# Performance work log

Hardware: AMD Instinct MI355X
Metric: run time of the kernel (lower is better)

## Reference

```python
import jax, jax.numpy as jnp
import numpy as np

# dims
B, C, LM, LE, D, R, P, M, NL = 64, 16, 40, 32, 768, 2048, 49, 4, 2
COS_EPS = 1e-8
# fixed graph topology from GCNLayer: vertexes = [mention_text, mention_image, entity_text, entity_image]
VERTEX_GRAPH = [[(0, 2), (1, 3)], [(2, 2), (3, 3)], [(0, 0), (2, 1)], [(1, 0), (3, 1)]]
EDGE_GRAPH = [(0, 2), (0, 3), (1, 2), (1, 3)]


def _cos(x, y):
    # torch.nn.CosineSimilarity(dim=-1): dot / max(|x|*|y|, eps)
    num = jnp.sum(x * y, axis=-1)
    den = jnp.sqrt(jnp.sum(x * x, axis=-1)) * jnp.sqrt(jnp.sum(y * y, axis=-1))
    return num / jnp.maximum(den, COS_EPS)


def _span_mean(feat, start, end):
    # mean of token features over [start, end] inclusive  (mention final repr)
    pos = jnp.arange(feat.shape[1])
    m = ((pos >= start[:, None]) & (pos <= end[:, None])).astype(feat.dtype)[..., None]
    return (feat * m).sum(1) / jnp.maximum(m.sum(1), 1e-9)


def _ln(x, g, b):
    mu = jnp.mean(x, axis=-1, keepdims=True)
    var = jnp.mean((x - mu) ** 2, axis=-1, keepdims=True)
    return (x - mu) / jnp.sqrt(var + 1e-5) * g + b


def setup_inputs() -> dict:
    key = jax.random.key(0)
    ks = jax.random.split(key, 32)
    n = lambda i, shape, s=1.0: jax.random.normal(ks[i], shape, jnp.float32) * s
    start = jax.random.randint(ks[20], (B,), 0, 16)
    end = start + jax.random.randint(ks[21], (B,), 1, 16)
    return {
        "mention_text_feature": n(0, (B, LM, D)),
        "mention_text_mask": jnp.ones((B, LM), jnp.int32),
        "mention_start_pos": start,
        "mention_end_pos": end,
        "mention_image_feature": n(1, (B, P, R)),
        "mention_object_feature": n(2, (B, M, R)),
        "mention_object_score": jax.random.uniform(ks[22], (B, M), jnp.float32),
        "entity_text_feature": n(3, (B, C, LE, D)),
        "entity_text_mask": jnp.ones((B, C, LE), jnp.int32),
        "entity_image_feature": n(4, (B, C, P, R)),
        "entity_object_feature": n(5, (B, C, M, R)),
        "entity_object_score": jax.random.uniform(ks[23], (B, C, M), jnp.float32),
        "miet_similarity": n(6, (B, C)),
        "mtei_similarity": n(7, (B, C)),
        "w_mt": n(8, (D, D), 0.02), "b_mt": jnp.zeros((D,), jnp.float32),
        "w_et": n(9, (D, D), 0.02), "b_et": jnp.zeros((D,), jnp.float32),
        "w_mi": n(10, (R, D), 0.02), "b_mi": jnp.zeros((D,), jnp.float32),
        "w_ei": n(11, (R, D), 0.02), "b_ei": jnp.zeros((D,), jnp.float32),
        "wh_w": n(12, (NL, D, D), 0.02), "wh_b": jnp.zeros((NL, D), jnp.float32),
        "wu_w": n(13, (NL, D, D), 0.02), "wu_b": jnp.zeros((NL, D), jnp.float32),
        "wv_w": n(14, (NL, D, D), 0.02), "wv_b": jnp.zeros((NL, D), jnp.float32),
        "ln_g": jnp.ones((NL, D), jnp.float32), "ln_b": jnp.zeros((NL, D), jnp.float32),
    }


def reference(mention_text_feature, mention_text_mask, mention_start_pos, mention_end_pos,
              mention_image_feature, mention_object_feature, mention_object_score,
              entity_text_feature, entity_text_mask, entity_image_feature,
              entity_object_feature, entity_object_score, miet_similarity, mtei_similarity,
              w_mt, b_mt, w_et, b_et, w_mi, b_mi, w_ei, b_ei,
              wh_w, wh_b, wu_w, wu_b, wv_w, wv_b, ln_g, ln_b):
    # ---------------- VertexEncoder ----------------
    span = _span_mean(mention_text_feature, mention_start_pos, mention_end_pos)        # [B, D]
    v0 = span @ w_mt + b_mt                                                            # mention text  [B, D]
    em = entity_text_mask.astype(jnp.float32)[..., None]                               # [B, C, LE, 1]
    ent_rep = (entity_text_feature * em).sum(2) / jnp.maximum(em.sum(2), 1e-9)         # [B, C, D]
    v2 = ent_rep @ w_et + b_et                                                         # entity text   [B, C, D]
    v1 = mention_image_feature.mean(1) @ w_mi + b_mi                                   # mention image [B, D]
    v3 = entity_image_feature.mean(2) @ w_ei + b_ei                                    # entity image  [B, C, D]
    # ---------------- EdgeEncoder ----------------
    mtet = _cos(span[:, None, :], entity_text_feature[:, :, 0])                        # [B, C]
    # pairwise object cosine: vectorized over the torch double loop
    dots = jnp.einsum('bmr,bcnr->bcmn', mention_object_feature, entity_object_feature)
    nm = jnp.sqrt(jnp.sum(mention_object_feature ** 2, -1))                            # [B, M]
    ne = jnp.sqrt(jnp.sum(entity_object_feature ** 2, -1))                             # [B, C, M]
    sim = dots / jnp.maximum(nm[:, None, :, None] * ne[:, :, None, :], COS_EPS)        # [B, C, M, M]
    score = mention_object_score[:, None, :, None] * entity_object_score[:, :, None, :]
    miei = (sim * score).sum((-2, -1)) / (score.sum((-2, -1)) + 1e-9)                  # [B, C]
    # scaler edges (gcn_edge_enabled = all ones)
    edges = [mtet, mtei_similarity / 100.0, miet_similarity / 100.0, miei]
    vertexes = [v0, v1, v2, v3]
    # ---------------- GCN layers ----------------
    def conv_v(e, v):
        # scaler edge e: [B, C];  v is [B, C, D] (entity) or [B, D] (mention)
        if v.ndim == 3:
            return jnp.mean(e[:, :, None] * v, axis=1)          # -> [B, D]
        return e[:, :, None] * v[:, None, :]                    # -> [B, C, D]

    for l in range(NL):
        wh, bh = wh_w[l], wh_b[l]
        wu, bu = wu_w[l], wu_b[l]
        wv, bv = wv_w[l], wv_b[l]
        g, bln = ln_g[l], ln_b[l]
        new_v = []
        for u, nbrs in zip(vertexes, VERTEX_GRAPH):
            s = u
            for ei, vi in nbrs:
                s = s + conv_v(edges[ei], vertexes[vi])
            new_v.append(jax.nn.relu(_ln(s @ wh + bh, g, bln)))
        new_e = []
        for e, (ui, vi) in zip(edges, EDGE_GRAPH):
            fu = (vertexes[ui] @ wu + bu)[:, None, :]           # [B, 1, D]
            fv = vertexes[vi] @ wv + bv                         # [B, C, D]
            ne2 = jnp.mean(fu * fv, axis=-1)                    # [B, C]
            new_e.append(jax.nn.relu(ne2 + e))                  # w_m = Identity in scaler mode
        vertexes, edges = new_v, new_e
    # ---------------- output ----------------
    return _cos(vertexes[0][:, None, :], vertexes[2])           # [B, C]
```

## Files before the change

kernel.cpp:

```cpp
#include <hip/hip_runtime.h>

#define DIMB 64
#define DIMC 16
#define DIMLM 40
#define DIMLE 32
#define DIMD 768
#define DIMR 2048
#define DIMP 49
#define BC (DIMB * DIMC)

typedef __attribute__((ext_vector_type(8))) short short8;
typedef __attribute__((ext_vector_type(4))) float f32x4;

__device__ __forceinline__ float warpSum(float v) {
  v += __shfl_down(v, 32); v += __shfl_down(v, 16); v += __shfl_down(v, 8);
  v += __shfl_down(v, 4);  v += __shfl_down(v, 2);  v += __shfl_down(v, 1);
  return v;
}

__device__ __forceinline__ float blockSum256(float v, float* buf) {
  v = warpSum(v);
  int lane = threadIdx.x & 63, wid = threadIdx.x >> 6;
  if (lane == 0) buf[wid] = v;
  __syncthreads();
  float s = buf[0] + buf[1] + buf[2] + buf[3];
  __syncthreads();
  return s;
}

__device__ __forceinline__ void splitf(float x, unsigned short& h, unsigned short& l) {
  unsigned bx = __float_as_uint(x);
  h = (unsigned short)(bx >> 16);
  float lo = x - __uint_as_float(bx & 0xffff0000u);
  unsigned bl = __float_as_uint(lo);
  l = (unsigned short)((bl + 0x7fffu + ((bl >> 16) & 1u)) >> 16);
}

__global__ void k_span(const float* __restrict__ mtf, const int* __restrict__ st,
                       const int* __restrict__ en, float* __restrict__ outp) {
  int b = blockIdx.x;
  int s = st[b], e = en[b];
  float cnt = 0.0f;
  for (int p = 0; p < DIMLM; ++p) cnt += (p >= s && p <= e) ? 1.0f : 0.0f;
  float den = fmaxf(cnt, 1e-9f);
  for (int d = threadIdx.x; d < DIMD; d += 256) {
    float acc = 0.0f;
    for (int p = s; p <= e && p < DIMLM; ++p)
      acc += mtf[((size_t)b * DIMLM + p) * DIMD + d];
    outp[b * DIMD + d] = acc / den;
  }
}

__global__ void k_entrep(const float* __restrict__ etf, const int* __restrict__ etm,
                         float* __restrict__ outp) {
  int bc = blockIdx.x;
  const float4* f = (const float4*)(etf + (size_t)bc * DIMLE * DIMD);
  const int* mk = etm + bc * DIMLE;
  float cnt = 0.0f;
  for (int l = 0; l < DIMLE; ++l) cnt += (float)mk[l];
  float rden = 1.0f / fmaxf(cnt, 1e-9f);
  for (int d4 = threadIdx.x; d4 < DIMD / 4; d4 += 256) {
    float sx = 0, sy = 0, sz = 0, sw = 0;
    for (int l = 0; l < DIMLE; ++l) {
      float m = (float)mk[l];
      float4 v = f[(size_t)l * (DIMD / 4) + d4];
      sx += v.x * m; sy += v.y * m; sz += v.z * m; sw += v.w * m;
    }
    float4 o = { sx * rden, sy * rden, sz * rden, sw * rden };
    ((float4*)(outp + (size_t)bc * DIMD))[d4] = o;
  }
}

__global__ void k_pmean(const float* __restrict__ in, float* __restrict__ outp, int np) {
  int row = blockIdx.y;
  int r4 = blockIdx.x * 256 + threadIdx.x;
  const float4* p = (const float4*)(in + (size_t)row * np * DIMR) + r4;
  float sx = 0, sy = 0, sz = 0, sw = 0;
  for (int i = 0; i < np; ++i) {
    float4 v = p[(size_t)i * (DIMR / 4)];
    sx += v.x; sy += v.y; sz += v.z; sw += v.w;
  }
  float rn = 1.0f / (float)np;
  float4 o = { sx * rn, sy * rn, sz * rn, sw * rn };
  ((float4*)(outp + (size_t)row * DIMR))[r4] = o;
}

__global__ void k_mtet(const float* __restrict__ span, const float* __restrict__ etf,
                       float* __restrict__ e0) {
  __shared__ float buf[4];
  int bc = blockIdx.x, b = bc >> 4;
  const float* x = span + b * DIMD;
  const float* y = etf + (size_t)bc * DIMLE * DIMD;
  float dot = 0, nx = 0, ny = 0;
  for (int d = threadIdx.x; d < DIMD; d += 256) {
    float xv = x[d], yv = y[d];
    dot += xv * yv; nx += xv * xv; ny += yv * yv;
  }
  dot = blockSum256(dot, buf);
  nx = blockSum256(nx, buf);
  ny = blockSum256(ny, buf);
  if (threadIdx.x == 0) e0[bc] = dot / fmaxf(sqrtf(nx) * sqrtf(ny), 1e-8f);
}

__global__ void k_einit(const float* __restrict__ mtei, const float* __restrict__ miet,
                        float* __restrict__ e1, float* __restrict__ e2) {
  int i = blockIdx.x * 256 + threadIdx.x;
  if (i < BC) { e1[i] = mtei[i] * 0.01f; e2[i] = miet[i] * 0.01f; }
}

__global__ void k_miei(const float* __restrict__ mof, const float* __restrict__ eof,
                       const float* __restrict__ mos, const float* __restrict__ eos,
                       float* __restrict__ e3) {
  __shared__ float red[24][4];
  int bc = blockIdx.x, b = bc >> 4;
  const float* mop = mof + (size_t)b * 4 * DIMR;
  const float* eop = eof + (size_t)bc * 4 * DIMR;
  float dots[16] = {}; float nm2[4] = {}; float ne2[4] = {};
  for (int r = threadIdx.x; r < DIMR; r += 256) {
    float mv[4], ev[4];
#pragma unroll
    for (int m = 0; m < 4; ++m) mv[m] = mop[(size_t)m * DIMR + r];
#pragma unroll
    for (int n = 0; n < 4; ++n) ev[n] = eop[(size_t)n * DIMR + r];
#pragma unroll
    for (int m = 0; m < 4; ++m) {
      nm2[m] += mv[m] * mv[m];
#pragma unroll
      for (int n = 0; n < 4; ++n) dots[m * 4 + n] += mv[m] * ev[n];
    }
#pragma unroll
    for (int n = 0; n < 4; ++n) ne2[n] += ev[n] * ev[n];
  }
  int lane = threadIdx.x & 63, wid = threadIdx.x >> 6;
#pragma unroll
  for (int i = 0; i < 24; ++i) {
    float v = (i < 16) ? dots[i] : (i < 20 ? nm2[i - 16] : ne2[i - 20]);
    v = warpSum(v);
    if (lane == 0) red[i][wid] = v;
  }
  __syncthreads();
  if (threadIdx.x == 0) {
    float dsum[16], nmv[4], nev[4];
    for (int i = 0; i < 16; ++i) dsum[i] = red[i][0] + red[i][1] + red[i][2] + red[i][3];
    for (int m = 0; m < 4; ++m)
      nmv[m] = sqrtf(red[16 + m][0] + red[16 + m][1] + red[16 + m][2] + red[16 + m][3]);
    for (int n = 0; n < 4; ++n)
      nev[n] = sqrtf(red[20 + n][0] + red[20 + n][1] + red[20 + n][2] + red[20 + n][3]);
    float num = 0, den = 0;
    for (int m = 0; m < 4; ++m)
      for (int n = 0; n < 4; ++n) {
        float sim = dsum[m * 4 + n] / fmaxf(nmv[m] * nev[n], 1e-8f);
        float sc = mos[b * 4 + m] * eos[bc * 4 + n];
        num += sim * sc; den += sc;
      }
    e3[bc] = num / (den + 1e-9f);
  }
}

struct WDesc { const float* W; unsigned short* Th; unsigned short* Tl; int K; };
struct WDescs { WDesc d[10]; };
__global__ void k_wsplitT(WDescs wd) {
  const WDesc D = wd.d[blockIdx.z];
  int kb = blockIdx.x * 32;
  if (kb >= D.K) return;
  int nb = blockIdx.y * 32;
  __shared__ float t[32][33];
  int c = threadIdx.x & 31, r8 = threadIdx.x >> 5;
#pragma unroll
  for (int i = 0; i < 4; ++i) {
    int kk = r8 + i * 8;
    t[kk][c] = D.W[(size_t)(kb + kk) * DIMD + nb + c];
  }
  __syncthreads();
#pragma unroll
  for (int i = 0; i < 4; ++i) {
    int nn = r8 + i * 8;
    unsigned short h, l;
    splitf(t[c][nn], h, l);
    size_t o = (size_t)(nb + nn) * D.K + kb + c;
    D.Th[o] = h; D.Tl[o] = l;
  }
}

struct ADesc { const float* X; unsigned short* H; unsigned short* L; };
struct ADescs { ADesc d[4]; int cum[5]; int nd; };
__global__ void k_asplit(ADescs ad) {
  int i4 = blockIdx.x * 256 + threadIdx.x;
  for (int z = 0; z < ad.nd; ++z) {
    if (i4 < ad.cum[z + 1]) {
      int off = i4 - ad.cum[z];
      const ADesc D = ad.d[z];
      float4 v = ((const float4*)D.X)[off];
      unsigned short h0, h1, h2, h3, l0, l1, l2, l3;
      splitf(v.x, h0, l0); splitf(v.y, h1, l1);
      splitf(v.z, h2, l2); splitf(v.w, h3, l3);
      uint2 hp, lp;
      hp.x = (unsigned)h0 | ((unsigned)h1 << 16); hp.y = (unsigned)h2 | ((unsigned)h3 << 16);
      lp.x = (unsigned)l0 | ((unsigned)l1 << 16); lp.y = (unsigned)l2 | ((unsigned)l3 << 16);
      ((uint2*)D.H)[off] = hp;
      ((uint2*)D.L)[off] = lp;
      return;
    }
  }
}

#define BMg 128
#define BNg 128
#define BKg 32
#define LDP 40
struct GDesc {
  const unsigned short *Ah, *Al, *Wh, *Wl;
  const float* bias; float* C; int M, K, mb0;
};
struct GDescs { GDesc d[4]; int nd; };

__global__ __launch_bounds__(256) void k_gemm_mfma(GDescs gd) {
  int bx = blockIdx.x;
  int z = 0;
  while (z + 1 < gd.nd && bx >= gd.d[z + 1].mb0) ++z;
  const GDesc D = gd.d[z];
  const int m0 = (bx - D.mb0) * BMg;
  const int n0 = blockIdx.y * BNg;
  const int K = D.K, M = D.M;

  __shared__ unsigned short sAh[2][BMg * LDP];
  __shared__ unsigned short sAl[2][BMg * LDP];
  __shared__ unsigned short sWh[2][BMg * LDP];
  __shared__ unsigned short sWl[2][BMg * LDP];

  const int tid = threadIdx.x;
  uint4 st[8];

  auto issue = [&](int kt) {
    int k0 = kt * BKg;
#pragma unroll
    for (int i = 0; i < 8; ++i) {
      int u = tid + (i & 1) * 256;
      int r = u >> 2, q = u & 3;
      const unsigned short* src;
      int row;
      if (i < 4) { row = m0 + r; if (row >= M) row = M - 1; src = (i < 2) ? D.Ah : D.Al; }
      else       { row = n0 + r;                            src = (i < 6) ? D.Wh : D.Wl; }
      st[i] = *(const uint4*)(src + (size_t)row * K + k0 + q * 8);
    }
  };
  auto commit = [&](int b) {
#pragma unroll
    for (int i = 0; i < 8; ++i) {
      int u = tid + (i & 1) * 256;
      int r = u >> 2, q = u & 3;
      unsigned short* dst = (i < 2) ? sAh[b] : (i < 4) ? sAl[b] : (i < 6) ? sWh[b] : sWl[b];
      *(uint4*)(dst + r * LDP + q * 8) = st[i];
    }
  };

  f32x4 acc[4][4];
#pragma unroll
  for (int i = 0; i < 4; ++i)
#pragma unroll
    for (int j = 0; j < 4; ++j) acc[i][j] = (f32x4){0.f, 0.f, 0.f, 0.f};

  const int lane = tid & 63, w = tid >> 6;
  const int wr = (w >> 1) * 64, wc = (w & 1) * 64;
  const int fr = lane & 15, fg = lane >> 4;

  issue(0); commit(0); __syncthreads();
  const int nt = K / BKg;
  for (int t = 0; t < nt; ++t) {
    int b = t & 1;
    if (t + 1 < nt) issue(t + 1);
    short8 ah[4], al[4];
#pragma unroll
    for (int mi = 0; mi < 4; ++mi) {
      int ro = (wr + mi * 16 + fr) * LDP + fg * 8;
      ah[mi] = *(const short8*)(sAh[b] + ro);
      al[mi] = *(const short8*)(sAl[b] + ro);
    }
#pragma unroll
    for (int ni = 0; ni < 4; ++ni) {
      int co = (wc + ni * 16 + fr) * LDP + fg * 8;
      short8 wh8 = *(const short8*)(sWh[b] + co);
      short8 wl8 = *(const short8*)(sWl[b] + co);
#pragma unroll
      for (int mi = 0; mi < 4; ++mi) {
        acc[mi][ni] = __builtin_amdgcn_mfma_f32_16x16x32_bf16(ah[mi], wh8, acc[mi][ni], 0, 0, 0);
        acc[mi][ni] = __builtin_amdgcn_mfma_f32_16x16x32_bf16(ah[mi], wl8, acc[mi][ni], 0, 0, 0);
        acc[mi][ni] = __builtin_amdgcn_mfma_f32_16x16x32_bf16(al[mi], wh8, acc[mi][ni], 0, 0, 0);
      }
    }
    if (t + 1 < nt) commit((t + 1) & 1);
    __syncthreads();
  }

#pragma unroll
  for (int mi = 0; mi < 4; ++mi) {
#pragma unroll
    for (int r = 0; r < 4; ++r) {
      int grow = m0 + wr + mi * 16 + fg * 4 + r;
      if (grow < M) {
#pragma unroll
        for (int ni = 0; ni < 4; ++ni) {
          int gcol = n0 + wc + ni * 16 + fr;
          D.C[(size_t)grow * DIMD + gcol] = acc[mi][ni][r] + D.bias[gcol];
        }
      }
    }
  }
}

__global__ void k_agg_m(const float* __restrict__ V, const float* __restrict__ e,
                        float* __restrict__ SC) {
  int b = blockIdx.x;
  const float* v0 = V;
  const float* v1 = V + 64 * DIMD;
  const float* v2 = V + 128 * DIMD;
  const float* v3 = V + 1152 * DIMD;
  for (int d = threadIdx.x; d < DIMD; d += 256) {
    float a0 = 0, a1 = 0;
    for (int c = 0; c < DIMC; ++c) {
      int bc = b * DIMC + c;
      float x2 = v2[(size_t)bc * DIMD + d], x3 = v3[(size_t)bc * DIMD + d];
      a0 += e[bc] * x2 + e[BC + bc] * x3;
      a1 += e[2 * BC + bc] * x2 + e[3 * BC + bc] * x3;
    }
    SC[(size_t)b * DIMD + d] = v0[b * DIMD + d] + a0 * (1.0f / DIMC);
    SC[(size_t)(64 + b) * DIMD + d] = v1[b * DIMD + d] + a1 * (1.0f / DIMC);
  }
}

__global__ void k_agg_e(const float* __restrict__ V, const float* __restrict__ e,
                        float* __restrict__ SC) {
  size_t i = (size_t)blockIdx.x * 256 + threadIdx.x;
  int d = (int)(i % DIMD);
  int bc = (int)(i / DIMD);
  int b = bc >> 4;
  const float* v0 = V;
  const float* v1 = V + 64 * DIMD;
  const float* v2 = V + 128 * DIMD;
  const float* v3 = V + 1152 * DIMD;
  float e0 = e[bc], e1 = e[BC + bc], e2v = e[2 * BC + bc], e3v = e[3 * BC + bc];
  float x0 = v0[b * DIMD + d], x1 = v1[b * DIMD + d];
  SC[(size_t)128 * DIMD + i] = v2[i] + e0 * x0 + e2v * x1;
  SC[(size_t)1152 * DIMD + i] = v3[i] + e1 * x0 + e3v * x1;
}

__global__ void k_ln_relu(float* __restrict__ x, const float* __restrict__ g,
                          const float* __restrict__ bb) {
  __shared__ float buf[4];
  float* xr = x + (size_t)blockIdx.x * DIMD;
  float v[3];
  float s = 0.0f;
#pragma unroll
  for (int i = 0; i < 3; ++i) { v[i] = xr[threadIdx.x + i * 256]; s += v[i]; }
  float mu = blockSum256(s, buf) / (float)DIMD;
  float q = 0.0f;
#pragma unroll
  for (int i = 0; i < 3; ++i) { float d = v[i] - mu; q += d * d; }
  float var = blockSum256(q, buf) / (float)DIMD;
  float inv = 1.0f / sqrtf(var + 1e-5f);
#pragma unroll
  for (int i = 0; i < 3; ++i) {
    int d = threadIdx.x + i * 256;
    float y = (v[i] - mu) * inv * g[d] + bb[d];
    xr[d] = fmaxf(y, 0.0f);
  }
}

__global__ void k_edge_upd(const float* __restrict__ FU, const float* __restrict__ FV,
                           const float* __restrict__ eold, float* __restrict__ enew) {
  __shared__ float buf[4];
  int bc = blockIdx.x, b = bc >> 4;
  const float* fu0 = FU;
  const float* fu1 = FU + 64 * DIMD;
  const float* fv2 = FV;
  const float* fv3 = FV + 1024 * DIMD;
  float d02 = 0, d03 = 0, d12 = 0, d13 = 0;
  for (int d = threadIdx.x; d < DIMD; d += 256) {
    float u0 = fu0[b * DIMD + d], u1 = fu1[b * DIMD + d];
    float w2 = fv2[(size_t)bc * DIMD + d], w3 = fv3[(size_t)bc * DIMD + d];
    d02 += u0 * w2; d03 += u0 * w3; d12 += u1 * w2; d13 += u1 * w3;
  }
  d02 = blockSum256(d02, buf);
  d03 = blockSum256(d03, buf);
  d12 = blockSum256(d12, buf);
  d13 = blockSum256(d13, buf);
  if (threadIdx.x == 0) {
    enew[bc]          = fmaxf(d02 / (float)DIMD + eold[bc], 0.0f);
    enew[BC + bc]     = fmaxf(d03 / (float)DIMD + eold[BC + bc], 0.0f);
    enew[2 * BC + bc] = fmaxf(d12 / (float)DIMD + eold[2 * BC + bc], 0.0f);
    enew[3 * BC + bc] = fmaxf(d13 / (float)DIMD + eold[3 * BC + bc], 0.0f);
  }
}

__global__ void k_out(const float* __restrict__ V, float* __restrict__ outp) {
  __shared__ float buf[4];
  int bc = blockIdx.x, b = bc >> 4;
  const float* nv0 = V;
  const float* nv2 = V + 128 * DIMD;
  float dot = 0, n0 = 0, n2 = 0;
  for (int d = threadIdx.x; d < DIMD; d += 256) {
    float x = nv0[b * DIMD + d], y = nv2[(size_t)bc * DIMD + d];
    dot += x * y; n0 += x * x; n2 += y * y;
  }
  dot = blockSum256(dot, buf);
  n0 = blockSum256(n0, buf);
  n2 = blockSum256(n2, buf);
  if (threadIdx.x == 0) outp[bc] = dot / fmaxf(sqrtf(n0) * sqrtf(n2), 1e-8f);
}

extern "C" void kernel_launch(void* const* d_in, const int* in_sizes, int n_in,
                              void* d_out, int out_size, void* d_ws, size_t ws_size,
                              hipStream_t stream) {
  const float* mtf    = (const float*)d_in[0];
  const int*   mstart = (const int*)d_in[2];
  const int*   mend   = (const int*)d_in[3];
  const float* mif  = (const float*)d_in[4];
  const float* mof  = (const float*)d_in[5];
  const float* mos  = (const float*)d_in[6];
  const float* etf  = (const float*)d_in[7];
  const int*   etm  = (const int*)d_in[8];
  const float* eif  = (const float*)d_in[9];
  const float* eof  = (const float*)d_in[10];
  const float* eos  = (const float*)d_in[11];
  const float* miet = (const float*)d_in[12];
  const float* mtei = (const float*)d_in[13];
  const float* w_mt = (const float*)d_in[14]; const float* b_mt = (const float*)d_in[15];
  const float* w_et = (const float*)d_in[16]; const float* b_et = (const float*)d_in[17];
  const float* w_mi = (const float*)d_in[18]; const float* b_mi = (const float*)d_in[19];
  const float* w_ei = (const float*)d_in[20]; const float* b_ei = (const float*)d_in[21];
  const float* wh_w = (const float*)d_in[22]; const float* wh_b = (const float*)d_in[23];
  const float* wu_w = (const float*)d_in[24]; const float* wu_b = (const float*)d_in[25];
  const float* wv_w = (const float*)d_in[26]; const float* wv_b = (const float*)d_in[27];
  const float* ln_g = (const float*)d_in[28]; const float* ln_b = (const float*)d_in[29];
  float* out = (float*)d_out;

  float* ws = (float*)d_ws;
  size_t off = 0;
  auto alloc = [&](size_t n) { float* p = ws + off; off += n; return p; };
  const size_t NV = 2176;
  float* span   = alloc((size_t)DIMB * DIMD);
  float* entrep = alloc((size_t)BC * DIMD);
  float* mimg   = alloc((size_t)DIMB * DIMR);
  float* eimg   = alloc((size_t)BC * DIMR);
  float* V[2]   = { alloc(NV * DIMD), alloc(NV * DIMD) };
  float* SCAT   = alloc(NV * DIMD);
  float* FU     = alloc((size_t)128 * DIMD);
  float* FV     = alloc((size_t)2048 * DIMD);
  float* ebuf[2] = { alloc((size_t)4 * BC), alloc((size_t)4 * BC) };

  unsigned short* us = (unsigned short*)(ws + off);
  size_t uoff = 0;
  auto ualloc = [&](size_t n) { unsigned short* p = us + uoff; uoff += n; return p; };
  unsigned short* sp_h = ualloc(64 * 768);   unsigned short* sp_l = ualloc(64 * 768);
  unsigned short* mi_h = ualloc(64 * 2048);  unsigned short* mi_l = ualloc(64 * 2048);
  unsigned short* en_h = ualloc(1024 * 768); unsigned short* en_l = ualloc(1024 * 768);
  unsigned short* ei_h = ualloc((size_t)1024 * 2048); unsigned short* ei_l = ualloc((size_t)1024 * 2048);
  unsigned short* sc_h = ualloc(NV * 768);   unsigned short* sc_l = ualloc(NV * 768);
  unsigned short* vv_h = ualloc(NV * 768);   unsigned short* vv_l = ualloc(NV * 768);
  unsigned short* wmtT_h = ualloc(768 * 768);  unsigned short* wmtT_l = ualloc(768 * 768);
  unsigned short* wetT_h = ualloc(768 * 768);  unsigned short* wetT_l = ualloc(768 * 768);
  unsigned short* wmiT_h = ualloc((size_t)768 * 2048); unsigned short* wmiT_l = ualloc((size_t)768 * 2048);
  unsigned short* weiT_h = ualloc((size_t)768 * 2048); unsigned short* weiT_l = ualloc((size_t)768 * 2048);
  unsigned short* whT_h[2] = { ualloc(768 * 768), ualloc(768 * 768) };
  unsigned short* whT_l[2] = { ualloc(768 * 768), ualloc(768 * 768) };
  unsigned short* wuT_h[2] = { ualloc(768 * 768), ualloc(768 * 768) };
  unsigned short* wuT_l[2] = { ualloc(768 * 768), ualloc(768 * 768) };
  unsigned short* wvT_h[2] = { ualloc(768 * 768), ualloc(768 * 768) };
  unsigned short* wvT_l[2] = { ualloc(768 * 768), ualloc(768 * 768) };

  k_span<<<DIMB, 256, 0, stream>>>(mtf, mstart, mend, span);
  k_entrep<<<BC, 256, 0, stream>>>(etf, etm, entrep);
  k_pmean<<<dim3(DIMR / 4 / 256, DIMB), 256, 0, stream>>>(mif, mimg, DIMP);
  k_pmean<<<dim3(DIMR / 4 / 256, BC), 256, 0, stream>>>(eif, eimg, DIMP);
  k_mtet<<<BC, 256, 0, stream>>>(span, etf, ebuf[0]);
  k_einit<<<(BC + 255) / 256, 256, 0, stream>>>(mtei, miet, ebuf[0] + BC, ebuf[0] + 2 * BC);
  k_miei<<<BC, 256, 0, stream>>>(mof, eof, mos, eos, ebuf[0] + 3 * BC);

  {
    WDescs wd;
    wd.d[0] = { w_mt, wmtT_h, wmtT_l, 768 };
    wd.d[1] = { w_et, wetT_h, wetT_l, 768 };
    wd.d[2] = { w_mi, wmiT_h, wmiT_l, 2048 };
    wd.d[3] = { w_ei, weiT_h, weiT_l, 2048 };
    wd.d[4] = { wh_w,             whT_h[0], whT_l[0], 768 };
    wd.d[5] = { wh_w + 768 * 768, whT_h[1], whT_l[1], 768 };
    wd.d[6] = { wu_w,             wuT_h[0], wuT_l[0], 768 };
    wd.d[7] = { wu_w + 768 * 768, wuT_h[1], wuT_l[1], 768 };
    wd.d[8] = { wv_w,             wvT_h[0], wvT_l[0], 768 };
    wd.d[9] = { wv_w + 768 * 768, wvT_h[1], wvT_l[1], 768 };
    k_wsplitT<<<dim3(2048 / 32, 768 / 32, 10), 256, 0, stream>>>(wd);
  }

  {
    ADescs ad;
    ad.nd = 4;
    ad.d[0] = { span,   sp_h, sp_l };
    ad.d[1] = { mimg,   mi_h, mi_l };
    ad.d[2] = { entrep, en_h, en_l };
    ad.d[3] = { eimg,   ei_h, ei_l };
    ad.cum[0] = 0;
    ad.cum[1] = 64 * 768 / 4;
    ad.cum[2] = ad.cum[1] + 64 * 2048 / 4;
    ad.cum[3] = ad.cum[2] + 1024 * 768 / 4;
    ad.cum[4] = ad.cum[3] + 1024 * 2048 / 4;
    k_asplit<<<(ad.cum[4] + 255) / 256, 256, 0, stream>>>(ad);
  }

  {
    GDescs gd;
    gd.nd = 4;
    gd.d[0] = { sp_h, sp_l, wmtT_h, wmtT_l, b_mt, V[0],               64,  768,  0 };
    gd.d[1] = { mi_h, mi_l, wmiT_h, wmiT_l, b_mi, V[0] + 64 * DIMD,   64,  2048, 1 };
    gd.d[2] = { en_h, en_l, wetT_h, wetT_l, b_et, V[0] + 128 * DIMD,  1024, 768, 2 };
    gd.d[3] = { ei_h, ei_l, weiT_h, weiT_l, b_ei, V[0] + 1152 * DIMD, 1024, 2048, 10 };
    k_gemm_mfma<<<dim3(18, 6), 256, 0, stream>>>(gd);
  }

  int cur = 0;
  for (int l = 0; l < 2; ++l) {
    int nxt = cur ^ 1;
    k_agg_m<<<DIMB, 256, 0, stream>>>(V[cur], ebuf[cur], SCAT);
    k_agg_e<<<(1024 * DIMD) / 256, 256, 0, stream>>>(V[cur], ebuf[cur], SCAT);
    {
      ADescs ad;
      ad.nd = 2;
      ad.d[0] = { SCAT,   sc_h, sc_l };
      ad.d[1] = { V[cur], vv_h, vv_l };
      ad.cum[0] = 0;
      ad.cum[1] = (int)(NV * 768 / 4);
      ad.cum[2] = (int)(2 * NV * 768 / 4);
      k_asplit<<<(ad.cum[2] + 255) / 256, 256, 0, stream>>>(ad);
    }
    {
      GDescs gd;
      gd.nd = 3;
      gd.d[0] = { sc_h, sc_l, whT_h[l], whT_l[l], wh_b + l * DIMD, V[nxt], (int)NV, 768, 0 };
      gd.d[1] = { vv_h, vv_l, wuT_h[l], wuT_l[l], wu_b + l * DIMD, FU, 128, 768, 17 };
      gd.d[2] = { vv_h + 128 * 768, vv_l + 128 * 768, wvT_h[l], wvT_l[l],
                  wv_b + l * DIMD, FV, 2048, 768, 18 };
      k_gemm_mfma<<<dim3(34, 6), 256, 0, stream>>>(gd);
    }
    k_ln_relu<<<(int)NV, 256, 0, stream>>>(V[nxt], ln_g + l * DIMD, ln_b + l * DIMD);
    k_edge_upd<<<BC, 256, 0, stream>>>(FU, FV, ebuf[cur], ebuf[nxt]);
    cur = nxt;
  }

  k_out<<<BC, 256, 0, stream>>>(V[cur], out);
}
```

Measured before the change: 1.140 ms.

## Fuse hi/lo bf16 split into producer kernels and merge aggregation passes

The reductions (span mean, entity text mean, patch means) now write the bf16 hi/lo split operands directly, so the fp32 intermediates and the separate split kernel are no longer needed. The two image mean launches become one, and the edge init is folded into k_mtet. Each layer's aggregation of mention and entity vertices and the split of both the aggregated and self features move into one vectorized kernel. This cuts launches and the global round trips of the fp32 intermediates, at the cost of a more branchy combined kernel with some redundant reads across the mention rows.

Result: faster. 1.090 ms (-4.4%).

```diff
diff --git a/kernel.cpp b/kernel.cpp
--- a/kernel.cpp
+++ b/kernel.cpp
@@ -8,6 +8,7 @@
 #define DIMR 2048
 #define DIMP 49
 #define BC (DIMB * DIMC)
+#define NV 2176
 
 typedef __attribute__((ext_vector_type(8))) short short8;
 typedef __attribute__((ext_vector_type(4))) float f32x4;
@@ -36,23 +37,38 @@
   l = (unsigned short)((bl + 0x7fffu + ((bl >> 16) & 1u)) >> 16);
 }
 
-__global__ void k_span(const float* __restrict__ mtf, const int* __restrict__ st,
-                       const int* __restrict__ en, float* __restrict__ outp) {
+__device__ __forceinline__ void split4(float4 o, uint2& hp, uint2& lp) {
+  unsigned short h0, h1, h2, h3, l0, l1, l2, l3;
+  splitf(o.x, h0, l0); splitf(o.y, h1, l1);
+  splitf(o.z, h2, l2); splitf(o.w, h3, l3);
+  hp.x = (unsigned)h0 | ((unsigned)h1 << 16); hp.y = (unsigned)h2 | ((unsigned)h3 << 16);
+  lp.x = (unsigned)l0 | ((unsigned)l1 << 16); lp.y = (unsigned)l2 | ((unsigned)l3 << 16);
+}
+
+__global__ void k_span_split(const float* __restrict__ mtf, const int* __restrict__ st,
+                             const int* __restrict__ en, float* __restrict__ spanf,
+                             unsigned short* __restrict__ H, unsigned short* __restrict__ L) {
   int b = blockIdx.x;
   int s = st[b], e = en[b];
   float cnt = 0.0f;
   for (int p = 0; p < DIMLM; ++p) cnt += (p >= s && p <= e) ? 1.0f : 0.0f;
-  float den = fmaxf(cnt, 1e-9f);
-  for (int d = threadIdx.x; d < DIMD; d += 256) {
-    float acc = 0.0f;
-    for (int p = s; p <= e && p < DIMLM; ++p)
-      acc += mtf[((size_t)b * DIMLM + p) * DIMD + d];
-    outp[b * DIMD + d] = acc / den;
-  }
-}
-
-__global__ void k_entrep(const float* __restrict__ etf, const int* __restrict__ etm,
-                         float* __restrict__ outp) {
+  float rden = 1.0f / fmaxf(cnt, 1e-9f);
+  for (int d4 = threadIdx.x; d4 < DIMD / 4; d4 += 256) {
+    float4 a = {0.f, 0.f, 0.f, 0.f};
+    for (int p = s; p <= e && p < DIMLM; ++p) {
+      float4 v = ((const float4*)(mtf + ((size_t)b * DIMLM + p) * DIMD))[d4];
+      a.x += v.x; a.y += v.y; a.z += v.z; a.w += v.w;
+    }
+    float4 o = { a.x * rden, a.y * rden, a.z * rden, a.w * rden };
+    ((float4*)(spanf + (size_t)b * DIMD))[d4] = o;
+    uint2 hp, lp; split4(o, hp, lp);
+    ((uint2*)H)[(size_t)b * (DIMD / 4) + d4] = hp;
+    ((uint2*)L)[(size_t)b * (DIMD / 4) + d4] = lp;
+  }
+}
+
+__global__ void k_entrep_split(const float* __restrict__ etf, const int* __restrict__ etm,
+                               unsigned short* __restrict__ H, unsigned short* __restrict__ L) {
   int bc = blockIdx.x;
   const float4* f = (const float4*)(etf + (size_t)bc * DIMLE * DIMD);
   const int* mk = etm + bc * DIMLE;
@@ -67,26 +83,37 @@
       sx += v.x * m; sy += v.y * m; sz += v.z * m; sw += v.w * m;
     }
     float4 o = { sx * rden, sy * rden, sz * rden, sw * rden };
-    ((float4*)(outp + (size_t)bc * DIMD))[d4] = o;
-  }
-}
-
-__global__ void k_pmean(const float* __restrict__ in, float* __restrict__ outp, int np) {
+    uint2 hp, lp; split4(o, hp, lp);
+    ((uint2*)H)[(size_t)bc * (DIMD / 4) + d4] = hp;
+    ((uint2*)L)[(size_t)bc * (DIMD / 4) + d4] = lp;
+  }
+}
+
+__global__ void k_pmean_split(const float* __restrict__ mif, const float* __restrict__ eif,
+                              unsigned short* __restrict__ mi_h, unsigned short* __restrict__ mi_l,
+                              unsigned short* __restrict__ ei_h, unsigned short* __restrict__ ei_l) {
   int row = blockIdx.y;
   int r4 = blockIdx.x * 256 + threadIdx.x;
-  const float4* p = (const float4*)(in + (size_t)row * np * DIMR) + r4;
+  const float* src; unsigned short *H, *L; int lr;
+  if (row < DIMB) { src = mif; H = mi_h; L = mi_l; lr = row; }
+  else            { src = eif; H = ei_h; L = ei_l; lr = row - DIMB; }
+  const float4* p = (const float4*)(src + (size_t)lr * DIMP * DIMR) + r4;
   float sx = 0, sy = 0, sz = 0, sw = 0;
-  for (int i = 0; i < np; ++i) {
+  for (int i = 0; i < DIMP; ++i) {
     float4 v = p[(size_t)i * (DIMR / 4)];
     sx += v.x; sy += v.y; sz += v.z; sw += v.w;
   }
-  float rn = 1.0f / (float)np;
+  const float rn = 1.0f / (float)DIMP;
   float4 o = { sx * rn, sy * rn, sz * rn, sw * rn };
-  ((float4*)(outp + (size_t)row * DIMR))[r4] = o;
+  uint2 hp, lp; split4(o, hp, lp);
+  ((uint2*)H)[(size_t)lr * (DIMR / 4) + r4] = hp;
+  ((uint2*)L)[(size_t)lr * (DIMR / 4) + r4] = lp;
 }
 
 __global__ void k_mtet(const float* __restrict__ span, const float* __restrict__ etf,
-                       float* __restrict__ e0) {
+                       const float* __restrict__ mtei, const float* __restrict__ miet,
+                       float* __restrict__ e0, float* __restrict__ e1,
+                       float* __restrict__ e2) {
   __shared__ float buf[4];
   int bc = blockIdx.x, b = bc >> 4;
   const float* x = span + b * DIMD;
@@ -100,12 +127,8 @@
   nx = blockSum256(nx, buf);
   ny = blockSum256(ny, buf);
   if (threadIdx.x == 0) e0[bc] = dot / fmaxf(sqrtf(nx) * sqrtf(ny), 1e-8f);
-}
-
-__global__ void k_einit(const float* __restrict__ mtei, const float* __restrict__ miet,
-                        float* __restrict__ e1, float* __restrict__ e2) {
-  int i = blockIdx.x * 256 + threadIdx.x;
-  if (i < BC) { e1[i] = mtei[i] * 0.01f; e2[i] = miet[i] * 0.01f; }
+  if (threadIdx.x == 1) e1[bc] = mtei[bc] * 0.01f;
+  if (threadIdx.x == 2) e2[bc] = miet[bc] * 0.01f;
 }
 
 __global__ void k_miei(const float* __restrict__ mof, const float* __restrict__ eof,
@@ -182,28 +205,6 @@
   }
 }
 
-struct ADesc { const float* X; unsigned short* H; unsigned short* L; };
-struct ADescs { ADesc d[4]; int cum[5]; int nd; };
-__global__ void k_asplit(ADescs ad) {
-  int i4 = blockIdx.x * 256 + threadIdx.x;
-  for (int z = 0; z < ad.nd; ++z) {
-    if (i4 < ad.cum[z + 1]) {
-      int off = i4 - ad.cum[z];
-      const ADesc D = ad.d[z];
-      float4 v = ((const float4*)D.X)[off];
-      unsigned short h0, h1, h2, h3, l0, l1, l2, l3;
-      splitf(v.x, h0, l0); splitf(v.y, h1, l1);
-      splitf(v.z, h2, l2); splitf(v.w, h3, l3);
-      uint2 hp, lp;
-      hp.x = (unsigned)h0 | ((unsigned)h1 << 16); hp.y = (unsigned)h2 | ((unsigned)h3 << 16);
-      lp.x = (unsigned)l0 | ((unsigned)l1 << 16); lp.y = (unsigned)l2 | ((unsigned)l3 << 16);
-      ((uint2*)D.H)[off] = hp;
-      ((uint2*)D.L)[off] = lp;
-      return;
-    }
-  }
-}
-
 #define BMg 128
 #define BNg 128
 #define BKg 32
@@ -308,40 +309,55 @@
   }
 }
 
-__global__ void k_agg_m(const float* __restrict__ V, const float* __restrict__ e,
-                        float* __restrict__ SC) {
-  int b = blockIdx.x;
-  const float* v0 = V;
-  const float* v1 = V + 64 * DIMD;
-  const float* v2 = V + 128 * DIMD;
-  const float* v3 = V + 1152 * DIMD;
-  for (int d = threadIdx.x; d < DIMD; d += 256) {
-    float a0 = 0, a1 = 0;
+__global__ void k_layer_pre(const float* __restrict__ V, const float* __restrict__ e,
+                            unsigned short* __restrict__ sc_h, unsigned short* __restrict__ sc_l,
+                            unsigned short* __restrict__ vv_h, unsigned short* __restrict__ vv_l) {
+  size_t i4 = (size_t)blockIdx.x * 256 + threadIdx.x;
+  int row = (int)(i4 / (DIMD / 4)), d4 = (int)(i4 % (DIMD / 4));
+  const float4* v0 = (const float4*)V;
+  const float4* v1 = v0 + (size_t)64 * (DIMD / 4);
+  const float4* v2 = v0 + (size_t)128 * (DIMD / 4);
+  const float4* v3 = v0 + (size_t)1152 * (DIMD / 4);
+
+  float4 vself = ((const float4*)V)[i4];
+  uint2 hp, lp; split4(vself, hp, lp);
+  ((uint2*)vv_h)[i4] = hp;
+  ((uint2*)vv_l)[i4] = lp;
+
+  float4 s;
+  if (row < 128) {
+    int b = row & 63;
+    int men = row >> 6;
+    const float* ea = e + (men ? 2 * BC : 0);
+    const float* eb_ = e + (men ? 3 * BC : BC);
+    float ax = 0, ay = 0, az = 0, aw = 0;
     for (int c = 0; c < DIMC; ++c) {
       int bc = b * DIMC + c;
-      float x2 = v2[(size_t)bc * DIMD + d], x3 = v3[(size_t)bc * DIMD + d];
-      a0 += e[bc] * x2 + e[BC + bc] * x3;
-      a1 += e[2 * BC + bc] * x2 + e[3 * BC + bc] * x3;
-    }
-    SC[(size_t)b * DIMD + d] = v0[b * DIMD + d] + a0 * (1.0f / DIMC);
-    SC[(size_t)(64 + b) * DIMD + d] = v1[b * DIMD + d] + a1 * (1.0f / DIMC);
-  }
-}
-
-__global__ void k_agg_e(const float* __restrict__ V, const float* __restrict__ e,
-                        float* __restrict__ SC) {
-  size_t i = (size_t)blockIdx.x * 256 + threadIdx.x;
-  int d = (int)(i % DIMD);
-  int bc = (int)(i / DIMD);
-  int b = bc >> 4;
-  const float* v0 = V;
-  const float* v1 = V + 64 * DIMD;
-  const float* v2 = V + 128 * DIMD;
-  const float* v3 = V + 1152 * DIMD;
-  float e0 = e[bc], e1 = e[BC + bc], e2v = e[2 * BC + bc], e3v = e[3 * BC + bc];
-  float x0 = v0[b * DIMD + d], x1 = v1[b * DIMD + d];
-  SC[(size_t)128 * DIMD + i] = v2[i] + e0 * x0 + e2v * x1;
-  SC[(size_t)1152 * DIMD + i] = v3[i] + e1 * x0 + e3v * x1;
+      float4 x2 = v2[(size_t)bc * (DIMD / 4) + d4];
+      float4 x3 = v3[(size_t)bc * (DIMD / 4) + d4];
+      float w2 = ea[bc], w3 = eb_[bc];
+      ax += w2 * x2.x + w3 * x3.x; ay += w2 * x2.y + w3 * x3.y;
+      az += w2 * x2.z + w3 * x3.z; aw += w2 * x2.w + w3 * x3.w;
+    }
+    float4 u = (men ? v1 : v0)[(size_t)b * (DIMD / 4) + d4];
+    const float inv = 1.0f / DIMC;
+    s.x = u.x + ax * inv; s.y = u.y + ay * inv;
+    s.z = u.z + az * inv; s.w = u.w + aw * inv;
+  } else {
+    int ent = (row >= 1152);
+    int bc = row - (ent ? 1152 : 128);
+    int b = bc >> 4;
+    float w0 = e[bc + (ent ? BC : 0)];
+    float w1 = e[bc + (ent ? 3 * BC : 2 * BC)];
+    float4 x0 = v0[(size_t)b * (DIMD / 4) + d4];
+    float4 x1 = v1[(size_t)b * (DIMD / 4) + d4];
+    float4 u = (ent ? v3 : v2)[(size_t)bc * (DIMD / 4) + d4];
+    s.x = u.x + w0 * x0.x + w1 * x1.x; s.y = u.y + w0 * x0.y + w1 * x1.y;
+    s.z = u.z + w0 * x0.z + w1 * x1.z; s.w = u.w + w0 * x0.w + w1 * x1.w;
+  }
+  split4(s, hp, lp);
+  ((uint2*)sc_h)[i4] = hp;
+  ((uint2*)sc_l)[i4] = lp;
 }
 
 __global__ void k_ln_relu(float* __restrict__ x, const float* __restrict__ g,
@@ -373,7 +389,7 @@
   const float* fu0 = FU;
   const float* fu1 = FU + 64 * DIMD;
   const float* fv2 = FV;
-  const float* fv3 = FV + 1024 * DIMD;
+  const float* fv3 = FV + (size_t)1024 * DIMD;
   float d02 = 0, d03 = 0, d12 = 0, d13 = 0;
   for (int d = threadIdx.x; d < DIMD; d += 256) {
     float u0 = fu0[b * DIMD + d], u1 = fu1[b * DIMD + d];
@@ -437,15 +453,10 @@
   float* ws = (float*)d_ws;
   size_t off = 0;
   auto alloc = [&](size_t n) { float* p = ws + off; off += n; return p; };
-  const size_t NV = 2176;
-  float* span   = alloc((size_t)DIMB * DIMD);
-  float* entrep = alloc((size_t)BC * DIMD);
-  float* mimg   = alloc((size_t)DIMB * DIMR);
-  float* eimg   = alloc((size_t)BC * DIMR);
-  float* V[2]   = { alloc(NV * DIMD), alloc(NV * DIMD) };
-  float* SCAT   = alloc(NV * DIMD);
-  float* FU     = alloc((size_t)128 * DIMD);
-  float* FV     = alloc((size_t)2048 * DIMD);
+  float* span  = alloc((size_t)DIMB * DIMD);
+  float* V[2]  = { alloc((size_t)NV * DIMD), alloc((size_t)NV * DIMD) };
+  float* FU    = alloc((size_t)128 * DIMD);
+  float* FV    = alloc((size_t)2048 * DIMD);
   float* ebuf[2] = { alloc((size_t)4 * BC), alloc((size_t)4 * BC) };
 
   unsigned short* us = (unsigned short*)(ws + off);
@@ -455,8 +466,8 @@
   unsigned short* mi_h = ualloc(64 * 2048);  unsigned short* mi_l = ualloc(64 * 2048);
   unsigned short* en_h = ualloc(1024 * 768); unsigned short* en_l = ualloc(1024 * 768);
   unsigned short* ei_h = ualloc((size_t)1024 * 2048); unsigned short* ei_l = ualloc((size_t)1024 * 2048);
-  unsigned short* sc_h = ualloc(NV * 768);   unsigned short* sc_l = ualloc(NV * 768);
-  unsigned short* vv_h = ualloc(NV * 768);   unsigned short* vv_l = ualloc(NV * 768);
+  unsigned short* sc_h = ualloc((size_t)NV * 768);   unsigned short* sc_l = ualloc((size_t)NV * 768);
+  unsigned short* vv_h = ualloc((size_t)NV * 768);   unsigned short* vv_l = ualloc((size_t)NV * 768);
   unsigned short* wmtT_h = ualloc(768 * 768);  unsigned short* wmtT_l = ualloc(768 * 768);
   unsigned short* wetT_h = ualloc(768 * 768);  unsigned short* wetT_l = ualloc(768 * 768);
   unsigned short* wmiT_h = ualloc((size_t)768 * 2048); unsigned short* wmiT_l = ualloc((size_t)768 * 2048);
@@ -468,12 +479,11 @@
   unsigned short* wvT_h[2] = { ualloc(768 * 768), ualloc(768 * 768) };
   unsigned short* wvT_l[2] = { ualloc(768 * 768), ualloc(768 * 768) };
 
-  k_span<<<DIMB, 256, 0, stream>>>(mtf, mstart, mend, span);
-  k_entrep<<<BC, 256, 0, stream>>>(etf, etm, entrep);
-  k_pmean<<<dim3(DIMR / 4 / 256, DIMB), 256, 0, stream>>>(mif, mimg, DIMP);
-  k_pmean<<<dim3(DIMR / 4 / 256, BC), 256, 0, stream>>>(eif, eimg, DIMP);
-  k_mtet<<<BC, 256, 0, stream>>>(span, etf, ebuf[0]);
-  k_einit<<<(BC + 255) / 256, 256, 0, stream>>>(mtei, miet, ebuf[0] + BC, ebuf[0] + 2 * BC);
+  k_span_split<<<DIMB, 256, 0, stream>>>(mtf, mstart, mend, span, sp_h, sp_l);
+  k_entrep_split<<<BC, 256, 0, stream>>>(etf, etm, en_h, en_l);
+  k_pmean_split<<<dim3(2, DIMB + BC), 256, 0, stream>>>(mif, eif, mi_h, mi_l, ei_h, ei_l);
+  k_mtet<<<BC, 256, 0, stream>>>(span, etf, mtei, miet,
+                                 ebuf[0], ebuf[0] + BC, ebuf[0] + 2 * BC);
   k_miei<<<BC, 256, 0, stream>>>(mof, eof, mos, eos, ebuf[0] + 3 * BC);
 
   {
@@ -492,26 +502,11 @@
   }
 
   {
-    ADescs ad;
-    ad.nd = 4;
-    ad.d[0] = { span,   sp_h, sp_l };
-    ad.d[1] = { mimg,   mi_h, mi_l };
-    ad.d[2] = { entrep, en_h, en_l };
-    ad.d[3] = { eimg,   ei_h, ei_l };
-    ad.cum[0] = 0;
-    ad.cum[1] = 64 * 768 / 4;
-    ad.cum[2] = ad.cum[1] + 64 * 2048 / 4;
-    ad.cum[3] = ad.cum[2] + 1024 * 768 / 4;
-    ad.cum[4] = ad.cum[3] + 1024 * 2048 / 4;
-    k_asplit<<<(ad.cum[4] + 255) / 256, 256, 0, stream>>>(ad);
-  }
-
-  {
     GDescs gd;
     gd.nd = 4;
-    gd.d[0] = { sp_h, sp_l, wmtT_h, wmtT_l, b_mt, V[0],               64,  768,  0 };
-    gd.d[1] = { mi_h, mi_l, wmiT_h, wmiT_l, b_mi, V[0] + 64 * DIMD,   64,  2048, 1 };
-    gd.d[2] = { en_h, en_l, wetT_h, wetT_l, b_et, V[0] + 128 * DIMD,  1024, 768, 2 };
+    gd.d[0] = { sp_h, sp_l, wmtT_h, wmtT_l, b_mt, V[0],               64,   768,  0 };
+    gd.d[1] = { mi_h, mi_l, wmiT_h, wmiT_l, b_mi, V[0] + 64 * DIMD,   64,   2048, 1 };
+    gd.d[2] = { en_h, en_l, wetT_h, wetT_l, b_et, V[0] + 128 * DIMD,  1024, 768,  2 };
     gd.d[3] = { ei_h, ei_l, weiT_h, weiT_l, b_ei, V[0] + 1152 * DIMD, 1024, 2048, 10 };
     k_gemm_mfma<<<dim3(18, 6), 256, 0, stream>>>(gd);
   }
@@ -519,28 +514,18 @@
   int cur = 0;
   for (int l = 0; l < 2; ++l) {
     int nxt = cur ^ 1;
-    k_agg_m<<<DIMB, 256, 0, stream>>>(V[cur], ebuf[cur], SCAT);
-    k_agg_e<<<(1024 * DIMD) / 256, 256, 0, stream>>>(V[cur], ebuf[cur], SCAT);
-    {
-      ADescs ad;
-      ad.nd = 2;
-      ad.d[0] = { SCAT,   sc_h, sc_l };
-      ad.d[1] = { V[cur], vv_h, vv_l };
-      ad.cum[0] = 0;
-      ad.cum[1] = (int)(NV * 768 / 4);
-      ad.cum[2] = (int)(2 * NV * 768 / 4);
-      k_asplit<<<(ad.cum[2] + 255) / 256, 256, 0, stream>>>(ad);
-    }
+    k_layer_pre<<<(NV * DIMD / 4) / 256, 256, 0, stream>>>(V[cur], ebuf[cur],
+                                                           sc_h, sc_l, vv_h, vv_l);
     {
       GDescs gd;
       gd.nd = 3;
-      gd.d[0] = { sc_h, sc_l, whT_h[l], whT_l[l], wh_b + l * DIMD, V[nxt], (int)NV, 768, 0 };
+      gd.d[0] = { sc_h, sc_l, whT_h[l], whT_l[l], wh_b + l * DIMD, V[nxt], NV, 768, 0 };
       gd.d[1] = { vv_h, vv_l, wuT_h[l], wuT_l[l], wu_b + l * DIMD, FU, 128, 768, 17 };
-      gd.d[2] = { vv_h + 128 * 768, vv_l + 128 * 768, wvT_h[l], wvT_l[l],
+      gd.d[2] = { vv_h + (size_t)128 * 768, vv_l + (size_t)128 * 768, wvT_h[l], wvT_l[l],
                   wv_b + l * DIMD, FV, 2048, 768, 18 };
       k_gemm_mfma<<<dim3(34, 6), 256, 0, stream>>>(gd);
     }
-    k_ln_relu<<<(int)NV, 256, 0, stream>>>(V[nxt], ln_g + l * DIMD, ln_b + l * DIMD);
+    k_ln_relu<<<NV, 256, 0, stream>>>(V[nxt], ln_g + l * DIMD, ln_b + l * DIMD);
     k_edge_upd<<<BC, 256, 0, stream>>>(FU, FV, ebuf[cur], ebuf[nxt]);
     cur = nxt;
   }
```
